# Kernel tuning notes

Measured on AMD Instinct MI355X. Metric: run time of the kernel, lower is better.

The kernel has to match this reference:

```python
import jax, jax.numpy as jnp
import numpy as np

DIM = 128
LAYERS = 3
N_NODES = 50000
N_EDGES = 640000
LN_EPS = 1e-5


def setup_inputs() -> dict:
    key = jax.random.key(0)
    ks = jax.random.split(key, 10)
    s = 1.0 / np.sqrt(DIM)
    x = jax.random.normal(ks[0], (N_NODES, DIM), dtype=jnp.float32)
    edge_index = jax.random.randint(ks[1], (2, N_EDGES), 0, N_NODES, dtype=jnp.int64)
    in_w = jax.random.uniform(ks[2], (DIM, DIM), jnp.float32, -s, s)
    in_b = jax.random.uniform(ks[3], (DIM,), jnp.float32, -s, s)
    w1 = jax.random.uniform(ks[4], (LAYERS, DIM, DIM), jnp.float32, -s, s)
    b1 = jax.random.uniform(ks[5], (LAYERS, DIM), jnp.float32, -s, s)
    w2 = jax.random.uniform(ks[6], (LAYERS, DIM, DIM), jnp.float32, -s, s)
    b2 = jax.random.uniform(ks[7], (LAYERS, DIM), jnp.float32, -s, s)
    ln_g = jnp.ones((LAYERS, DIM), jnp.float32)
    ln_b = jnp.zeros((LAYERS, DIM), jnp.float32)
    return {"x": x, "edge_index": edge_index, "in_w": in_w, "in_b": in_b,
            "w1": w1, "b1": b1, "w2": w2, "b2": b2, "ln_g": ln_g, "ln_b": ln_b}


def _layer_norm(z, g, b):
    mu = jnp.mean(z, axis=-1, keepdims=True)
    var = jnp.mean(jnp.square(z - mu), axis=-1, keepdims=True)
    return (z - mu) * jax.lax.rsqrt(var + LN_EPS) * g + b


def reference(x, edge_index, in_w, in_b, w1, b1, w2, b2, ln_g, ln_b):
    src, dst = edge_index[0], edge_index[1]
    n = x.shape[0]
    # degree is identical every layer in the original; compute once (same math)
    deg = jax.ops.segment_sum(jnp.ones(dst.shape, x.dtype), dst, num_segments=n)
    deg = jnp.maximum(deg, 1.0)[:, None]  # [N,1]
    h = x @ in_w + in_b  # [N,D]
    for i in range(w1.shape[0]):
        m = jax.ops.segment_sum(h[src], dst, num_segments=n) / deg  # gather+scatter
        mlp = jax.nn.relu(m @ w1[i] + b1[i]) @ w2[i] + b2[i]
        h = _layer_norm(h + mlp, ln_g[i], ln_b[i])
    return h
```

## Files before the change

### kernel.cpp

```cpp
#include <hip/hip_runtime.h>
#include <hip/hip_fp8.h>

#define DIM 128
#define LN_EPS 1e-5f
#define ECAP 640

typedef __attribute__((ext_vector_type(8))) short s16x8;
typedef __attribute__((ext_vector_type(4))) float f32x4;
typedef __attribute__((ext_vector_type(2))) float f32x2;
typedef __attribute__((ext_vector_type(4))) unsigned int u32x4;
typedef __attribute__((ext_vector_type(2))) unsigned int u32x2;

__device__ __forceinline__ unsigned short f2bf(float f) {
    unsigned u = __float_as_uint(f);
    unsigned r = u + 0x7fffu + ((u >> 16) & 1u);
    return (unsigned short)(r >> 16);
}
__device__ __forceinline__ float bf2f(unsigned short b) {
    return __uint_as_float(((unsigned)b) << 16);
}
__device__ __forceinline__ unsigned char f2fp8(float f) {
    return (unsigned char)__hip_cvt_float_to_fp8(f, __HIP_SATFINITE, __HIP_E4M3);
}
__device__ __forceinline__ void acc_fp8x4(float* a, unsigned v) {
    f32x2 lo = __builtin_amdgcn_cvt_pk_f32_fp8(v, false);
    f32x2 hi = __builtin_amdgcn_cvt_pk_f32_fp8(v, true);
    a[0] += lo[0]; a[1] += lo[1]; a[2] += hi[0]; a[3] += hi[1];
}
__device__ __forceinline__ void acc_fp8x16(float* a, u32x4 v) {
    acc_fp8x4(a + 0,  v[0]);
    acc_fp8x4(a + 4,  v[1]);
    acc_fp8x4(a + 8,  v[2]);
    acc_fp8x4(a + 12, v[3]);
}


__global__ void count_deg(const int* __restrict__ dst, int E, int* __restrict__ counts) {
    int i = (blockIdx.x * 256 + threadIdx.x) * 4;
    if (i + 3 < E) {
        int4 d = *(const int4*)(dst + i);
        atomicAdd(&counts[d.x], 1);
        atomicAdd(&counts[d.y], 1);
        atomicAdd(&counts[d.z], 1);
        atomicAdd(&counts[d.w], 1);
    } else {
        for (int j = i; j < E; ++j) atomicAdd(&counts[dst[j]], 1);
    }
}

__global__ __launch_bounds__(256) void scan_partials(const int* __restrict__ counts, int n,
                                                     int* __restrict__ bsum) {
    int base = blockIdx.x * 1024 + threadIdx.x * 4;
    int s = 0;
#pragma unroll
    for (int j = 0; j < 4; ++j) {
        int i = base + j;
        if (i < n) s += counts[i];
    }
#pragma unroll
    for (int off = 32; off > 0; off >>= 1) s += __shfl_xor(s, off, 64);
    __shared__ int wsum[4];
    int lane = threadIdx.x & 63, wid = threadIdx.x >> 6;
    if (lane == 0) wsum[wid] = s;
    __syncthreads();
    if (threadIdx.x == 0) bsum[blockIdx.x] = wsum[0] + wsum[1] + wsum[2] + wsum[3];
}

__global__ __launch_bounds__(64) void scan_bsums(const int* __restrict__ bsum,
                                                 int* __restrict__ bofs, int nb,
                                                 int* __restrict__ rowptr, int N, int E) {
    int lane = threadIdx.x;
    int carry = 0;
    for (int base = 0; base < nb; base += 64) {
        int v = (base + lane < nb) ? bsum[base + lane] : 0;
        int incl = v;
#pragma unroll
        for (int off = 1; off < 64; off <<= 1) {
            int t = __shfl_up(incl, off, 64);
            if (lane >= off) incl += t;
        }
        if (base + lane < nb) bofs[base + lane] = carry + incl - v;
        carry += __shfl(incl, 63, 64);
    }
    if (lane == 0) rowptr[N] = E;
}

__global__ __launch_bounds__(256) void scan_final(const int* __restrict__ counts, int n,
                                                  const int* __restrict__ bofs,
                                                  int* __restrict__ rowptr,
                                                  int* __restrict__ cursor,
                                                  float* __restrict__ dinv) {
    int base = blockIdx.x * 1024 + threadIdx.x * 4;
    int v[4];
#pragma unroll
    for (int j = 0; j < 4; ++j) {
        int i = base + j;
        v[j] = (i < n) ? counts[i] : 0;
    }
    int tsum = v[0] + v[1] + v[2] + v[3];
    int lane = threadIdx.x & 63, wid = threadIdx.x >> 6;
    int incl = tsum;
#pragma unroll
    for (int off = 1; off < 64; off <<= 1) {
        int t = __shfl_up(incl, off, 64);
        if (lane >= off) incl += t;
    }
    __shared__ int wsum[4];
    if (lane == 63) wsum[wid] = incl;
    __syncthreads();
    int wofs = 0;
    for (int w = 0; w < 4; ++w)
        if (w < wid) wofs += wsum[w];
    int excl = bofs[blockIdx.x] + wofs + (incl - tsum);
#pragma unroll
    for (int j = 0; j < 4; ++j) {
        int i = base + j;
        if (i < n) {
            rowptr[i] = excl;
            cursor[i] = excl;
            dinv[i] = 1.0f / (float)((v[j] > 1) ? v[j] : 1);
            excl += v[j];
        }
    }
}

__global__ void fill_csr(const int* __restrict__ src, const int* __restrict__ dst, int E,
                         int* __restrict__ cursor, int* __restrict__ srcidx) {
    int i = (blockIdx.x * 256 + threadIdx.x) * 4;
    if (i + 3 < E) {
        int4 s = *(const int4*)(src + i);
        int4 d = *(const int4*)(dst + i);
        int p0 = atomicAdd(&cursor[d.x], 1); srcidx[p0] = s.x;
        int p1 = atomicAdd(&cursor[d.y], 1); srcidx[p1] = s.y;
        int p2 = atomicAdd(&cursor[d.z], 1); srcidx[p2] = s.z;
        int p3 = atomicAdd(&cursor[d.w], 1); srcidx[p3] = s.w;
    } else {
        for (int j = i; j < E; ++j) {
            int p = atomicAdd(&cursor[dst[j]], 1);
            srcidx[p] = src[j];
        }
    }
}


__global__ __launch_bounds__(256) void cvt_weights(const float* __restrict__ in_w,
                                                   const float* __restrict__ w1,
                                                   const float* __restrict__ w2,
                                                   unsigned short* __restrict__ wt, int L) {
    int mat = blockIdx.x >> 3, part = blockIdx.x & 7;
    const float* src;
    if (mat == 0) src = in_w;
    else if (mat <= L) src = w1 + (size_t)(mat - 1) * DIM * DIM;
    else src = w2 + (size_t)(mat - 1 - L) * DIM * DIM;
    unsigned short* dst = wt + (size_t)mat * DIM * DIM;
    int base = part * 2048 + threadIdx.x;
#pragma unroll
    for (int j = 0; j < 8; ++j) {
        int i = base + j * 256;
        int k = i >> 7, n = i & 127;
        dst[n * DIM + k] = f2bf(src[i]);
    }
}


__global__ __launch_bounds__(256) void gemm_bias_mfma(const float* __restrict__ x,
                                                      const unsigned short* __restrict__ Wt,
                                                      const float* __restrict__ bias,
                                                      unsigned short* __restrict__ hb,
                                                      unsigned char* __restrict__ h8, int N) {
    int tid = threadIdx.x;
    int s = tid >> 6, lane = tid & 63;
    int quad = lane >> 4, l16 = lane & 15;
    int r0 = blockIdx.x * 16;
    int cs = s * 32;
    int arow = r0 + l16;
    bool av = arow < N;

    f32x4 acc[2];
    acc[0] = (f32x4){0.f, 0.f, 0.f, 0.f};
    acc[1] = (f32x4){0.f, 0.f, 0.f, 0.f};

    const float4* xp = (const float4*)(x + ((size_t)(av ? arow : 0) << 7)) + quad * 2;
#pragma unroll
    for (int k0 = 0; k0 < 128; k0 += 32) {
        s16x8 a = {0, 0, 0, 0, 0, 0, 0, 0};
        if (av) {
            float4 f0 = xp[k0 / 4];
            float4 f1 = xp[k0 / 4 + 1];
            a[0] = (short)f2bf(f0.x); a[1] = (short)f2bf(f0.y);
            a[2] = (short)f2bf(f0.z); a[3] = (short)f2bf(f0.w);
            a[4] = (short)f2bf(f1.x); a[5] = (short)f2bf(f1.y);
            a[6] = (short)f2bf(f1.z); a[7] = (short)f2bf(f1.w);
        }
        s16x8 b0 = *(const s16x8*)(Wt + ((size_t)(cs + l16) << 7) + quad * 8 + k0);
        s16x8 b1 = *(const s16x8*)(Wt + ((size_t)(cs + 16 + l16) << 7) + quad * 8 + k0);
        acc[0] = __builtin_amdgcn_mfma_f32_16x16x32_bf16(a, b0, acc[0], 0, 0, 0);
        acc[1] = __builtin_amdgcn_mfma_f32_16x16x32_bf16(a, b1, acc[1], 0, 0, 0);
    }

#pragma unroll
    for (int c = 0; c < 2; ++c) {
        int col = cs + c * 16 + l16;
        float bv = bias[col];
#pragma unroll
        for (int reg = 0; reg < 4; ++reg) {
            int grow = r0 + quad * 4 + reg;
            if (grow < N) {
                float o = acc[c][reg] + bv;
                hb[((size_t)grow << 7) + col] = f2bf(o);
                h8[((size_t)grow << 7) + col] = f2fp8(o);
            }
        }
    }
}


__global__ __launch_bounds__(256) void agg_mlp_ln(const unsigned short* __restrict__ hin,
                                                  const unsigned char* __restrict__ h8in,
                                                  const int* __restrict__ rowptr,
                                                  const int* __restrict__ srcidx,
                                                  const float* __restrict__ dinv,
                                                  const unsigned short* __restrict__ W1t,
                                                  const float* __restrict__ B1,
                                                  const unsigned short* __restrict__ W2t,
                                                  const float* __restrict__ B2,
                                                  const float* __restrict__ G,
                                                  const float* __restrict__ Bb,
                                                  unsigned short* __restrict__ hout,
                                                  unsigned char* __restrict__ h8out,
                                                  float* __restrict__ out_f32, int N) {
    __shared__ unsigned short M[32][132];
    __shared__ unsigned short P[32][132];
    __shared__ float s1p[4][32], s2p[4][32];
    __shared__ int eL[ECAP];
    __shared__ int rp[33];

    int tid = threadIdx.x;
    int w = tid >> 6, lane = tid & 63;
    int quad = lane >> 4, l16 = lane & 15;
    int g = lane >> 3, li = lane & 7;
    int r0 = blockIdx.x * 32;
    int cs = w * 32;

    if (tid < 33) {
        int idx = r0 + tid;
        rp[tid] = rowptr[idx < N ? idx : N];
    }
    __syncthreads();
    int ebase = rp[0];
    int etot = rp[32] - ebase;
    int estg = etot < ECAP ? etot : ECAP;
    for (int i = tid; i < estg; i += 256) eL[i] = srcidx[ebase + i];
    __syncthreads();

    int nrow = w * 8 + g;
    int nd = r0 + nrow;
    bool nv = nd < N;
    int ls = rp[nrow] - ebase;
    int le = rp[nrow + 1] - ebase;
    if (!nv) { ls = 0; le = 0; }
    float di = nv ? dinv[nd] : 0.f;

    const unsigned char* hsl = h8in + li * 16;

    float a[16];
#pragma unroll
    for (int j = 0; j < 16; ++j) a[j] = 0.f;

#define LIDX(jj) (((jj) < le) ? (((jj) < ECAP) ? eL[(jj)] : srcidx[ebase + (jj)]) : -1)

    int jA = ls;
    int iA0 = LIDX(jA + 0), iA1 = LIDX(jA + 1), iA2 = LIDX(jA + 2), iA3 = LIDX(jA + 3);
    u32x4 A0 = {0, 0, 0, 0}, A1 = {0, 0, 0, 0}, A2 = {0, 0, 0, 0}, A3 = {0, 0, 0, 0};
    if (iA0 >= 0) A0 = *(const u32x4*)(hsl + ((size_t)iA0 << 7));
    if (iA1 >= 0) A1 = *(const u32x4*)(hsl + ((size_t)iA1 << 7));
    if (iA2 >= 0) A2 = *(const u32x4*)(hsl + ((size_t)iA2 << 7));
    if (iA3 >= 0) A3 = *(const u32x4*)(hsl + ((size_t)iA3 << 7));
    int jB = jA + 4;
    int iB0 = LIDX(jB + 0), iB1 = LIDX(jB + 1), iB2 = LIDX(jB + 2), iB3 = LIDX(jB + 3);

    while (__any(jA < le)) {
        u32x4 B0 = {0, 0, 0, 0}, B1v = {0, 0, 0, 0}, B2v = {0, 0, 0, 0}, B3 = {0, 0, 0, 0};
        if (iB0 >= 0) B0  = *(const u32x4*)(hsl + ((size_t)iB0 << 7));
        if (iB1 >= 0) B1v = *(const u32x4*)(hsl + ((size_t)iB1 << 7));
        if (iB2 >= 0) B2v = *(const u32x4*)(hsl + ((size_t)iB2 << 7));
        if (iB3 >= 0) B3  = *(const u32x4*)(hsl + ((size_t)iB3 << 7));
        int jC = jB + 4;
        int iC0 = LIDX(jC + 0), iC1 = LIDX(jC + 1), iC2 = LIDX(jC + 2), iC3 = LIDX(jC + 3);
        acc_fp8x16(a, A0);
        acc_fp8x16(a, A1);
        acc_fp8x16(a, A2);
        acc_fp8x16(a, A3);
        jA = jB; A0 = B0; A1 = B1v; A2 = B2v; A3 = B3;
        jB = jC; iB0 = iC0; iB1 = iC1; iB2 = iC2; iB3 = iC3;
    }
#undef LIDX

    {
        u32x4 o0, o1;
#pragma unroll
        for (int j = 0; j < 4; ++j) {
            unsigned lo0 = f2bf(a[2 * j]     * di);
            unsigned hi0 = f2bf(a[2 * j + 1] * di);
            o0[j] = lo0 | (hi0 << 16);
            unsigned lo1 = f2bf(a[8 + 2 * j]     * di);
            unsigned hi1 = f2bf(a[8 + 2 * j + 1] * di);
            o1[j] = lo1 | (hi1 << 16);
        }
        *(u32x4*)(&M[nrow][li * 16])     = o0;
        *(u32x4*)(&M[nrow][li * 16 + 8]) = o1;
    }
    __syncthreads();

    unsigned short hvr[2][2][4];
#pragma unroll
    for (int rt = 0; rt < 2; ++rt) {
#pragma unroll
        for (int c = 0; c < 2; ++c) {
            int col = cs + c * 16 + l16;
#pragma unroll
            for (int reg = 0; reg < 4; ++reg) {
                int grow = r0 + rt * 16 + quad * 4 + reg;
                hvr[rt][c][reg] = (grow < N) ? hin[((size_t)grow << 7) + col] : (unsigned short)0;
            }
        }
    }

    f32x4 ac1[2][2];
    ac1[0][0] = (f32x4){0.f, 0.f, 0.f, 0.f}; ac1[0][1] = (f32x4){0.f, 0.f, 0.f, 0.f};
    ac1[1][0] = (f32x4){0.f, 0.f, 0.f, 0.f}; ac1[1][1] = (f32x4){0.f, 0.f, 0.f, 0.f};
#pragma unroll
    for (int k0 = 0; k0 < 128; k0 += 32) {
        s16x8 b0 = *(const s16x8*)(W1t + ((size_t)(cs + l16) << 7) + quad * 8 + k0);
        s16x8 b1 = *(const s16x8*)(W1t + ((size_t)(cs + 16 + l16) << 7) + quad * 8 + k0);
        s16x8 a0 = *(const s16x8*)(&M[l16][quad * 8 + k0]);
        s16x8 a1 = *(const s16x8*)(&M[16 + l16][quad * 8 + k0]);
        ac1[0][0] = __builtin_amdgcn_mfma_f32_16x16x32_bf16(a0, b0, ac1[0][0], 0, 0, 0);
        ac1[0][1] = __builtin_amdgcn_mfma_f32_16x16x32_bf16(a0, b1, ac1[0][1], 0, 0, 0);
        ac1[1][0] = __builtin_amdgcn_mfma_f32_16x16x32_bf16(a1, b0, ac1[1][0], 0, 0, 0);
        ac1[1][1] = __builtin_amdgcn_mfma_f32_16x16x32_bf16(a1, b1, ac1[1][1], 0, 0, 0);
    }
#pragma unroll
    for (int rt = 0; rt < 2; ++rt) {
#pragma unroll
        for (int c = 0; c < 2; ++c) {
            int col = cs + c * 16 + l16;
            float bv = B1[col];
#pragma unroll
            for (int reg = 0; reg < 4; ++reg) {
                float v = fmaxf(ac1[rt][c][reg] + bv, 0.f);
                P[rt * 16 + quad * 4 + reg][col] = f2bf(v);
            }
        }
    }
    __syncthreads();

    f32x4 ac2[2][2];
    ac2[0][0] = (f32x4){0.f, 0.f, 0.f, 0.f}; ac2[0][1] = (f32x4){0.f, 0.f, 0.f, 0.f};
    ac2[1][0] = (f32x4){0.f, 0.f, 0.f, 0.f}; ac2[1][1] = (f32x4){0.f, 0.f, 0.f, 0.f};
#pragma unroll
    for (int k0 = 0; k0 < 128; k0 += 32) {
        s16x8 b0 = *(const s16x8*)(W2t + ((size_t)(cs + l16) << 7) + quad * 8 + k0);
        s16x8 b1 = *(const s16x8*)(W2t + ((size_t)(cs + 16 + l16) << 7) + quad * 8 + k0);
        s16x8 a0 = *(const s16x8*)(&P[l16][quad * 8 + k0]);
        s16x8 a1 = *(const s16x8*)(&P[16 + l16][quad * 8 + k0]);
        ac2[0][0] = __builtin_amdgcn_mfma_f32_16x16x32_bf16(a0, b0, ac2[0][0], 0, 0, 0);
        ac2[0][1] = __builtin_amdgcn_mfma_f32_16x16x32_bf16(a0, b1, ac2[0][1], 0, 0, 0);
        ac2[1][0] = __builtin_amdgcn_mfma_f32_16x16x32_bf16(a1, b0, ac2[1][0], 0, 0, 0);
        ac2[1][1] = __builtin_amdgcn_mfma_f32_16x16x32_bf16(a1, b1, ac2[1][1], 0, 0, 0);
    }

    float z[2][2][4];
    float ps1[2][4] = {{0, 0, 0, 0}, {0, 0, 0, 0}};
    float ps2[2][4] = {{0, 0, 0, 0}, {0, 0, 0, 0}};
#pragma unroll
    for (int rt = 0; rt < 2; ++rt) {
#pragma unroll
        for (int c = 0; c < 2; ++c) {
            int col = cs + c * 16 + l16;
            float b2v = B2[col];
#pragma unroll
            for (int reg = 0; reg < 4; ++reg) {
                float hv = bf2f(hvr[rt][c][reg]);
                float zz = ac2[rt][c][reg] + b2v + hv;
                z[rt][c][reg] = zz;
                ps1[rt][reg] += zz;
                ps2[rt][reg] += zz * zz;
            }
        }
    }
#pragma unroll
    for (int off = 1; off < 16; off <<= 1) {
#pragma unroll
        for (int rt = 0; rt < 2; ++rt) {
#pragma unroll
            for (int reg = 0; reg < 4; ++reg) {
                ps1[rt][reg] += __shfl_xor(ps1[rt][reg], off, 64);
                ps2[rt][reg] += __shfl_xor(ps2[rt][reg], off, 64);
            }
        }
    }
    if (l16 == 0) {
#pragma unroll
        for (int rt = 0; rt < 2; ++rt) {
#pragma unroll
            for (int reg = 0; reg < 4; ++reg) {
                s1p[w][rt * 16 + quad * 4 + reg] = ps1[rt][reg];
                s2p[w][rt * 16 + quad * 4 + reg] = ps2[rt][reg];
            }
        }
    }
    __syncthreads();

#pragma unroll
    for (int rt = 0; rt < 2; ++rt) {
#pragma unroll
        for (int reg = 0; reg < 4; ++reg) {
            int row = rt * 16 + quad * 4 + reg;
            float S1 = s1p[0][row] + s1p[1][row] + s1p[2][row] + s1p[3][row];
            float S2 = s2p[0][row] + s2p[1][row] + s2p[2][row] + s2p[3][row];
            float mean = S1 * (1.0f / 128.0f);
            float var = S2 * (1.0f / 128.0f) - mean * mean;
            float rs = rsqrtf(var + LN_EPS);
            int grow = r0 + row;
            if (grow < N) {
#pragma unroll
                for (int c = 0; c < 2; ++c) {
                    int col = cs + c * 16 + l16;
                    float o = (z[rt][c][reg] - mean) * rs * G[col] + Bb[col];
                    if (out_f32) {
                        out_f32[((size_t)grow << 7) + col] = o;
                    } else {
                        hout[((size_t)grow << 7) + col] = f2bf(o);
                        h8out[((size_t)grow << 7) + col] = f2fp8(o);
                    }
                }
            }
        }
    }
}


extern "C" void kernel_launch(void* const* d_in, const int* in_sizes, int n_in,
                              void* d_out, int out_size, void* d_ws, size_t ws_size,
                              hipStream_t stream) {
    const float* x    = (const float*)d_in[0];
    const int*   ei   = (const int*)d_in[1];
    const float* in_w = (const float*)d_in[2];
    const float* in_b = (const float*)d_in[3];
    const float* w1   = (const float*)d_in[4];
    const float* b1   = (const float*)d_in[5];
    const float* w2   = (const float*)d_in[6];
    const float* b2   = (const float*)d_in[7];
    const float* ln_g = (const float*)d_in[8];
    const float* ln_b = (const float*)d_in[9];

    const int N = in_sizes[0] / DIM;
    const int E = in_sizes[1] / 2;
    const int LAYERS = in_sizes[4] / (DIM * DIM);

    const int* e_src = ei;
    const int* e_dst = ei + E;

    char* ws = (char*)d_ws;
    unsigned short* hb0    = (unsigned short*)ws;  ws += (size_t)N * DIM * 2;
    unsigned short* hb1    = (unsigned short*)ws;  ws += (size_t)N * DIM * 2;
    unsigned char*  h8a    = (unsigned char*)ws;   ws += (size_t)N * DIM;
    unsigned char*  h8b    = (unsigned char*)ws;   ws += (size_t)N * DIM;
    int*            counts = (int*)ws;             ws += (size_t)N * 4;
    int*            rowptr = (int*)ws;             ws += (size_t)(N + 1) * 4;
    int*            cursor = (int*)ws;             ws += (size_t)N * 4;
    float*          dinv   = (float*)ws;           ws += (size_t)N * 4;
    int*            srcidx = (int*)ws;             ws += (size_t)E * 4;
    int*            bsum   = (int*)ws;             ws += 4096;
    int*            bofs   = (int*)ws;             ws += 4096;
    unsigned short* wt     = (unsigned short*)ws;  ws += (size_t)(2 * LAYERS + 1) * DIM * DIM * 2;

    const int nScanBlocks = (N + 1023) / 1024;
    const int nMat = 2 * LAYERS + 1;

    (void)hipMemsetAsync(counts, 0, (size_t)N * 4, stream);
    count_deg<<<(E + 1023) / 1024, 256, 0, stream>>>(e_dst, E, counts);
    scan_partials<<<nScanBlocks, 256, 0, stream>>>(counts, N, bsum);
    scan_bsums<<<1, 64, 0, stream>>>(bsum, bofs, nScanBlocks, rowptr, N, E);
    scan_final<<<nScanBlocks, 256, 0, stream>>>(counts, N, bofs, rowptr, cursor, dinv);
    fill_csr<<<(E + 1023) / 1024, 256, 0, stream>>>(e_src, e_dst, E, cursor, srcidx);
    cvt_weights<<<nMat * 8, 256, 0, stream>>>(in_w, w1, w2, wt, LAYERS);

    const unsigned short* in_wt = wt;
    const unsigned short* w1t   = wt + (size_t)DIM * DIM;
    const unsigned short* w2t   = wt + (size_t)(1 + LAYERS) * DIM * DIM;

    gemm_bias_mfma<<<(N + 15) / 16, 256, 0, stream>>>(x, in_wt, in_b, hb0, h8a, N);

    int agg_grid = (N + 31) / 32;
    unsigned short* hin  = hb0;  unsigned char* h8in  = h8a;
    unsigned short* hout = hb1;  unsigned char* h8out = h8b;
    for (int i = 0; i < LAYERS; ++i) {
        float* out = (i == LAYERS - 1) ? (float*)d_out : nullptr;
        agg_mlp_ln<<<agg_grid, 256, 0, stream>>>(hin, h8in, rowptr, srcidx, dinv,
                                                 w1t + (size_t)i * DIM * DIM, b1 + (size_t)i * DIM,
                                                 w2t + (size_t)i * DIM * DIM, b2 + (size_t)i * DIM,
                                                 ln_g + (size_t)i * DIM, ln_b + (size_t)i * DIM,
                                                 hout, h8out, out, N);
        unsigned short* t = hin; hin = hout; hout = t;
        unsigned char* t8 = h8in; h8in = h8out; h8out = t8;
    }
}
```

Baseline: 357.8 us.

## Split fused aggregation+MLP+LayerNorm kernel into separate aggregate and MLP kernels

Un-fuses the per-layer kernel into an aggregate kernel that gathers fp8 neighbor rows and writes the mean message to a global bf16 buffer, and an mlp_ln kernel that reads it back into shared memory for the MFMA MLP and LayerNorm. The aggregate kernel uses no shared memory and no block-wide staging of edge indices, so it can run at higher occupancy, hiding gather latency better. In exchange it adds an N×128 bf16 round trip through global memory and one extra launch per layer, and drops the LDS-staged source index list.

Measured after the change: 335.4 us. 1.07x faster.

```diff
diff --git a/kernel.cpp b/kernel.cpp
--- a/kernel.cpp
+++ b/kernel.cpp
@@ -3,7 +3,6 @@
 
 #define DIM 128
 #define LN_EPS 1e-5f
-#define ECAP 640
 
 typedef __attribute__((ext_vector_type(8))) short s16x8;
 typedef __attribute__((ext_vector_type(4))) float f32x4;
@@ -215,50 +214,19 @@
 }
 
 
-__global__ __launch_bounds__(256) void agg_mlp_ln(const unsigned short* __restrict__ hin,
-                                                  const unsigned char* __restrict__ h8in,
-                                                  const int* __restrict__ rowptr,
-                                                  const int* __restrict__ srcidx,
-                                                  const float* __restrict__ dinv,
-                                                  const unsigned short* __restrict__ W1t,
-                                                  const float* __restrict__ B1,
-                                                  const unsigned short* __restrict__ W2t,
-                                                  const float* __restrict__ B2,
-                                                  const float* __restrict__ G,
-                                                  const float* __restrict__ Bb,
-                                                  unsigned short* __restrict__ hout,
-                                                  unsigned char* __restrict__ h8out,
-                                                  float* __restrict__ out_f32, int N) {
-    __shared__ unsigned short M[32][132];
-    __shared__ unsigned short P[32][132];
-    __shared__ float s1p[4][32], s2p[4][32];
-    __shared__ int eL[ECAP];
-    __shared__ int rp[33];
-
+__global__ __launch_bounds__(256) void aggregate(const unsigned char* __restrict__ h8in,
+                                                 const int* __restrict__ rowptr,
+                                                 const int* __restrict__ srcidx,
+                                                 const float* __restrict__ dinv,
+                                                 unsigned short* __restrict__ mout, int N) {
     int tid = threadIdx.x;
     int w = tid >> 6, lane = tid & 63;
-    int quad = lane >> 4, l16 = lane & 15;
     int g = lane >> 3, li = lane & 7;
-    int r0 = blockIdx.x * 32;
-    int cs = w * 32;
-
-    if (tid < 33) {
-        int idx = r0 + tid;
-        rp[tid] = rowptr[idx < N ? idx : N];
-    }
-    __syncthreads();
-    int ebase = rp[0];
-    int etot = rp[32] - ebase;
-    int estg = etot < ECAP ? etot : ECAP;
-    for (int i = tid; i < estg; i += 256) eL[i] = srcidx[ebase + i];
-    __syncthreads();
-
-    int nrow = w * 8 + g;
-    int nd = r0 + nrow;
+    int nd = blockIdx.x * 32 + w * 8 + g;
     bool nv = nd < N;
-    int ls = rp[nrow] - ebase;
-    int le = rp[nrow + 1] - ebase;
-    if (!nv) { ls = 0; le = 0; }
+
+    int e  = nv ? rowptr[nd] : 0;
+    int ee = nv ? rowptr[nd + 1] : 0;
     float di = nv ? dinv[nd] : 0.f;
 
     const unsigned char* hsl = h8in + li * 16;
@@ -267,26 +235,25 @@
 #pragma unroll
     for (int j = 0; j < 16; ++j) a[j] = 0.f;
 
-#define LIDX(jj) (((jj) < le) ? (((jj) < ECAP) ? eL[(jj)] : srcidx[ebase + (jj)]) : -1)
-
-    int jA = ls;
-    int iA0 = LIDX(jA + 0), iA1 = LIDX(jA + 1), iA2 = LIDX(jA + 2), iA3 = LIDX(jA + 3);
+#define GIDX(jj) (((jj) < ee) ? srcidx[(jj)] : -1)
+    int jA = e;
+    int iA0 = GIDX(jA + 0), iA1 = GIDX(jA + 1), iA2 = GIDX(jA + 2), iA3 = GIDX(jA + 3);
     u32x4 A0 = {0, 0, 0, 0}, A1 = {0, 0, 0, 0}, A2 = {0, 0, 0, 0}, A3 = {0, 0, 0, 0};
     if (iA0 >= 0) A0 = *(const u32x4*)(hsl + ((size_t)iA0 << 7));
     if (iA1 >= 0) A1 = *(const u32x4*)(hsl + ((size_t)iA1 << 7));
     if (iA2 >= 0) A2 = *(const u32x4*)(hsl + ((size_t)iA2 << 7));
     if (iA3 >= 0) A3 = *(const u32x4*)(hsl + ((size_t)iA3 << 7));
     int jB = jA + 4;
-    int iB0 = LIDX(jB + 0), iB1 = LIDX(jB + 1), iB2 = LIDX(jB + 2), iB3 = LIDX(jB + 3);
-
-    while (__any(jA < le)) {
+    int iB0 = GIDX(jB + 0), iB1 = GIDX(jB + 1), iB2 = GIDX(jB + 2), iB3 = GIDX(jB + 3);
+
+    while (__any(jA < ee)) {
         u32x4 B0 = {0, 0, 0, 0}, B1v = {0, 0, 0, 0}, B2v = {0, 0, 0, 0}, B3 = {0, 0, 0, 0};
         if (iB0 >= 0) B0  = *(const u32x4*)(hsl + ((size_t)iB0 << 7));
         if (iB1 >= 0) B1v = *(const u32x4*)(hsl + ((size_t)iB1 << 7));
         if (iB2 >= 0) B2v = *(const u32x4*)(hsl + ((size_t)iB2 << 7));
         if (iB3 >= 0) B3  = *(const u32x4*)(hsl + ((size_t)iB3 << 7));
         int jC = jB + 4;
-        int iC0 = LIDX(jC + 0), iC1 = LIDX(jC + 1), iC2 = LIDX(jC + 2), iC3 = LIDX(jC + 3);
+        int iC0 = GIDX(jC + 0), iC1 = GIDX(jC + 1), iC2 = GIDX(jC + 2), iC3 = GIDX(jC + 3);
         acc_fp8x16(a, A0);
         acc_fp8x16(a, A1);
         acc_fp8x16(a, A2);
@@ -294,9 +261,9 @@
         jA = jB; A0 = B0; A1 = B1v; A2 = B2v; A3 = B3;
         jB = jC; iB0 = iC0; iB1 = iC1; iB2 = iC2; iB3 = iC3;
     }
-#undef LIDX
-
-    {
+#undef GIDX
+
+    if (nv) {
         u32x4 o0, o1;
 #pragma unroll
         for (int j = 0; j < 4; ++j) {
@@ -307,8 +274,42 @@
             unsigned hi1 = f2bf(a[8 + 2 * j + 1] * di);
             o1[j] = lo1 | (hi1 << 16);
         }
-        *(u32x4*)(&M[nrow][li * 16])     = o0;
-        *(u32x4*)(&M[nrow][li * 16 + 8]) = o1;
+        unsigned short* mp = mout + ((size_t)nd << 7) + li * 16;
+        *(u32x4*)(mp)     = o0;
+        *(u32x4*)(mp + 8) = o1;
+    }
+}
+
+
+__global__ __launch_bounds__(256) void mlp_ln(const unsigned short* __restrict__ hin,
+                                              const unsigned short* __restrict__ m,
+                                              const unsigned short* __restrict__ W1t,
+                                              const float* __restrict__ B1,
+                                              const unsigned short* __restrict__ W2t,
+                                              const float* __restrict__ B2,
+                                              const float* __restrict__ G,
+                                              const float* __restrict__ Bb,
+                                              unsigned short* __restrict__ hout,
+                                              unsigned char* __restrict__ h8out,
+                                              float* __restrict__ out_f32, int N) {
+    __shared__ unsigned short M[32][132];
+    __shared__ unsigned short P[32][132];
+    __shared__ float s1p[4][32], s2p[4][32];
+
+    int tid = threadIdx.x;
+    int w = tid >> 6, lane = tid & 63;
+    int quad = lane >> 4, l16 = lane & 15;
+    int r0 = blockIdx.x * 32;
+    int cs = w * 32;
+
+#pragma unroll
+    for (int cc = 0; cc < 2; ++cc) {
+        int c = tid + cc * 256;
+        int row = c >> 4, colc = (c & 15) * 8;
+        int grow = r0 + row;
+        u32x4 v = {0, 0, 0, 0};
+        if (grow < N) v = *(const u32x4*)(m + ((size_t)grow << 7) + colc);
+        *(u32x4*)(&M[row][colc]) = v;
     }
     __syncthreads();
 
@@ -475,6 +476,7 @@
     int*            bsum   = (int*)ws;             ws += 4096;
     int*            bofs   = (int*)ws;             ws += 4096;
     unsigned short* wt     = (unsigned short*)ws;  ws += (size_t)(2 * LAYERS + 1) * DIM * DIM * 2;
+    unsigned short* mbuf   = (unsigned short*)ws;  ws += (size_t)N * DIM * 2;
 
     const int nScanBlocks = (N + 1023) / 1024;
     const int nMat = 2 * LAYERS + 1;
@@ -493,16 +495,17 @@
 
     gemm_bias_mfma<<<(N + 15) / 16, 256, 0, stream>>>(x, in_wt, in_b, hb0, h8a, N);
 
-    int agg_grid = (N + 31) / 32;
+    int tile_grid = (N + 31) / 32;
     unsigned short* hin  = hb0;  unsigned char* h8in  = h8a;
     unsigned short* hout = hb1;  unsigned char* h8out = h8b;
     for (int i = 0; i < LAYERS; ++i) {
         float* out = (i == LAYERS - 1) ? (float*)d_out : nullptr;
-        agg_mlp_ln<<<agg_grid, 256, 0, stream>>>(hin, h8in, rowptr, srcidx, dinv,
-                                                 w1t + (size_t)i * DIM * DIM, b1 + (size_t)i * DIM,
-                                                 w2t + (size_t)i * DIM * DIM, b2 + (size_t)i * DIM,
-                                                 ln_g + (size_t)i * DIM, ln_b + (size_t)i * DIM,
-                                                 hout, h8out, out, N);
+        aggregate<<<tile_grid, 256, 0, stream>>>(h8in, rowptr, srcidx, dinv, mbuf, N);
+        mlp_ln<<<tile_grid, 256, 0, stream>>>(hin, mbuf,
+                                              w1t + (size_t)i * DIM * DIM, b1 + (size_t)i * DIM,
+                                              w2t + (size_t)i * DIM * DIM, b2 + (size_t)i * DIM,
+                                              ln_g + (size_t)i * DIM, ln_b + (size_t)i * DIM,
+                                              hout, h8out, out, N);
         unsigned short* t = hin; hin = hout; hout = t;
         unsigned char* t8 = h8in; h8in = h8out; h8out = t8;
     }
```
